# Kernel optimization log

Hardware: AMD Instinct MI355X
Metric: run time of the kernel (lower is better)

## Reference

```python
import jax, jax.numpy as jnp
import numpy as np

H = 16
DH = 64


def setup_inputs() -> dict:
    key = jax.random.key(0)
    ks = jax.random.split(key, 8)
    b, n, m, d = 2, 2048, 2048, 1024
    inner = H * DH  # 1024
    return {
        "x": jax.random.normal(ks[0], (b, n, d), jnp.float32),
        "mem_k": jax.random.normal(ks[1], (b, m, inner), jnp.float32),
        "mem_v": jax.random.normal(ks[2], (b, m, inner), jnp.float32),
        "Wq": jax.random.normal(ks[3], (d, inner), jnp.float32) * (d ** -0.5),
        "Wkv": jax.random.normal(ks[4], (d, 2 * inner), jnp.float32) * (d ** -0.5),
        "b_kv": jax.random.normal(ks[5], (2 * inner,), jnp.float32) * 0.02,
        "Wo": jax.random.normal(ks[6], (inner, d), jnp.float32) * (inner ** -0.5),
        "b_o": jax.random.normal(ks[7], (d,), jnp.float32) * 0.02,
    }


def reference(x, mem_k, mem_v, Wq, Wkv, b_kv, Wo, b_o):
    b, n, d = x.shape
    scale = DH ** -0.5
    q = (x @ Wq) * scale                       # [b, n, h*dh]
    self_k, self_v = jnp.split(x @ Wkv + b_kv, 2, axis=-1)
    k = jnp.concatenate([mem_k, self_k], axis=1)   # [b, j, h*dh]
    v = jnp.concatenate([mem_v, self_v], axis=1)

    def split_heads(t):
        return t.reshape(b, t.shape[1], H, DH).transpose(0, 2, 1, 3)  # b h n d

    q, k, v = map(split_heads, (q, k, v))
    sim = jnp.einsum('bhid,bhjd->bhij', q, k)  # [b, h, n, j]
    i, j = sim.shape[-2:]
    # causal mask: query i may attend to keys up to position (j - i) + i
    causal_mask = jnp.triu(jnp.ones((i, j), dtype=bool), k=j - i + 1)
    mask_value = -jnp.finfo(sim.dtype).max
    sim = jnp.where(causal_mask[None, None], mask_value, sim)
    attn = jax.nn.softmax(sim, axis=-1)
    out = jnp.einsum('bhij,bhjd->bhid', attn, v)
    out = out.transpose(0, 2, 1, 3).reshape(b, n, H * DH)
    return out @ Wo + b_o
```

## Files before the change

### kernel.cpp

```cpp
#include <hip/hip_runtime.h>
#include <stdint.h>

typedef __bf16 bf16x8 __attribute__((ext_vector_type(8)));
typedef _Float16 f16x8 __attribute__((ext_vector_type(8)));
typedef float f32x4 __attribute__((ext_vector_type(4)));
typedef float f32x16 __attribute__((ext_vector_type(16)));

constexpr int Mm = 2048;
constexpr float QSCALE = 0.18033688011112042f;

__device__ __forceinline__ float exp2_fast(float x) {
  return __builtin_amdgcn_exp2f(x);
}

__device__ __forceinline__ uint16_t f2bf(float f) {
  union { float f; uint32_t u; } v; v.f = f;
  return (uint16_t)((v.u + 0x7FFFu + ((v.u >> 16) & 1u)) >> 16);
}
__device__ __forceinline__ uint32_t pack2(float a, float b) {
  return (uint32_t)f2bf(a) | ((uint32_t)f2bf(b) << 16);
}
__device__ __forceinline__ uint32_t pkrtz(float a, float b) {
  auto h2 = __builtin_amdgcn_cvt_pkrtz(a, b);
  return __builtin_bit_cast(uint32_t, h2);
}
__device__ __forceinline__ uint16_t f2h(float f) {
  _Float16 h = (_Float16)f;
  return __builtin_bit_cast(uint16_t, h);
}

__device__ __forceinline__ void async16(const void* g, void* l) {
  __builtin_amdgcn_global_load_lds(
      (__attribute__((address_space(1))) uint32_t*)g,
      (__attribute__((address_space(3))) uint32_t*)l, 16, 0, 0);
}

__device__ __forceinline__ bf16x8 frag64(const uint16_t* base, int row, int chunk) {
  return *(const bf16x8*)(base + row * 64 + chunk * 8);
}
__device__ __forceinline__ f16x8 frag64h(const uint16_t* base, int row, int chunk) {
  return *(const f16x8*)(base + row * 64 + chunk * 8);
}

__global__ __launch_bounds__(256) void prep_kernel(
    const float* __restrict__ x, const float* __restrict__ mem_k,
    const float* __restrict__ mem_v, const float* __restrict__ Wq,
    const float* __restrict__ Wkv, const float* __restrict__ Wo,
    uint16_t* __restrict__ Xb, uint16_t* __restrict__ WallT,
    uint16_t* __restrict__ WoT, uint16_t* __restrict__ Kh,
    uint16_t* __restrict__ VhT) {
  __shared__ float tile[64][65];
  __shared__ uint16_t vtile[64 * 66];
  const int tid = threadIdx.x;
  int blk = blockIdx.x;

  if (blk < 1024) {
    const float4* x4 = (const float4*)x;
    for (int it = 0; it < 4; ++it) {
      int idx4 = blk * 1024 + it * 256 + tid;
      float4 v = x4[idx4];
      uint2 w; w.x = pack2(v.x, v.y); w.y = pack2(v.z, v.w);
      ((uint2*)Xb)[idx4] = w;
    }
    return;
  }
  blk -= 1024;
  if (blk < 1024) {
    const float* src; uint16_t* dst; int ld, colbase, n0, k0;
    if (blk < 768) {
      int nt = blk >> 4, kt = blk & 15;
      n0 = nt * 64; k0 = kt * 64;
      if (n0 < 1024) { src = Wq; ld = 1024; colbase = n0; }
      else           { src = Wkv; ld = 2048; colbase = n0 - 1024; }
      dst = WallT;
    } else {
      int b2 = blk - 768;
      int nt = b2 >> 4, kt = b2 & 15;
      n0 = nt * 64; k0 = kt * 64;
      src = Wo; ld = 1024; colbase = n0; dst = WoT;
    }
    int r = tid >> 4, c = (tid & 15) * 4;
    for (int it = 0; it < 4; ++it) {
      int rr = r + it * 16;
      float4 v = *(const float4*)(src + (size_t)(k0 + rr) * ld + colbase + c);
      tile[rr][c] = v.x; tile[rr][c + 1] = v.y;
      tile[rr][c + 2] = v.z; tile[rr][c + 3] = v.w;
    }
    __syncthreads();
    for (int it = 0; it < 4; ++it) {
      int rn = r + it * 16;
      uint2 w;
      w.x = pack2(tile[c][rn], tile[c + 1][rn]);
      w.y = pack2(tile[c + 2][rn], tile[c + 3][rn]);
      *(uint2*)(dst + (size_t)(n0 + rn) * 1024 + k0 + c) = w;
    }
    return;
  }
  blk -= 1024;
  if (blk < 1024) {
    const float4* s4 = (const float4*)mem_k;
    for (int it = 0; it < 4; ++it) {
      int idx4 = blk * 1024 + it * 256 + tid;
      int e = idx4 * 4;
      int b = e >> 21;
      int rem = e & ((1 << 21) - 1);
      int m = rem >> 10;
      int cc = rem & 1023;
      int h = cc >> 6, dh = cc & 63;
      float4 v = s4[idx4];
      uint2 w; w.x = pack2(v.x, v.y); w.y = pack2(v.z, v.w);
      *(uint2*)(Kh + (((size_t)(b * 16 + h) * 4096) + m) * 64 + dh) = w;
    }
    return;
  }
  blk -= 1024;
  {
    const int b = blk >> 9, h = (blk >> 5) & 15, m0 = (blk & 31) * 64;
    const float4* s4 = (const float4*)mem_v;
    for (int it = 0; it < 4; ++it) {
      int idx = it * 256 + tid;
      int r = idx >> 4, d4 = (idx & 15) * 4;
      float4 v = s4[(size_t)(b * 2048 + m0 + r) * 256 + h * 16 + (d4 >> 2)];
      *(uint32_t*)&vtile[r * 66 + d4]     = pkrtz(v.x, v.y);
      *(uint32_t*)&vtile[r * 66 + d4 + 2] = pkrtz(v.z, v.w);
    }
    __syncthreads();
    int d = tid & 63;
    for (int half = 0; half < 2; ++half) {
      int mg = (tid >> 6) + half * 4;
      uint32_t w[4];
      for (int p = 0; p < 4; ++p) {
        uint32_t lo = vtile[(mg * 8 + 2 * p) * 66 + d];
        uint32_t hi = vtile[(mg * 8 + 2 * p + 1) * 66 + d];
        w[p] = lo | (hi << 16);
      }
      *(uint4*)&VhT[((size_t)((b * 16 + h) * 64) + d) * 4096 + m0 + mg * 8] =
          *(uint4*)w;
    }
  }
}

template <int MODE>
__global__ __launch_bounds__(256) void gemm_kernel(
    const uint16_t* __restrict__ A, const uint16_t* __restrict__ Bt,
    const float* __restrict__ bias, uint16_t* __restrict__ Qh,
    uint16_t* __restrict__ Kh, uint16_t* __restrict__ VhT,
    float* __restrict__ Out) {
  constexpr int K = 1024;
  constexpr int SS = 136;
  const int m0 = blockIdx.x * 128, n0 = blockIdx.y * 128;
  const int tid = threadIdx.x;
  const int wave = tid >> 6, lane = tid & 63;
  const int lhi = lane >> 4, llo = lane & 15;
  const int wm = (wave >> 1) * 64, wn = (wave & 1) * 64;

  __shared__ uint16_t sh[MODE == 0 ? 128 * SS : 128 * 128];
  uint16_t* As = sh;
  uint16_t* Bs = sh + 128 * 64;

  f32x4 acc[4][4] = {};

  for (int kt = 0; kt < K / 64; ++kt) {
    __syncthreads();
    for (int c = 0; c < 4; ++c) {
      int cl = (wave * 4 + c) * 64 + lane;
      int row = cl >> 3;
      int ch = cl & 7;
      async16(A + (size_t)(m0 + row) * K + kt * 64 + ch * 8, As + cl * 8);
      async16(Bt + (size_t)(n0 + row) * K + kt * 64 + ch * 8, Bs + cl * 8);
    }
    __syncthreads();
    for (int ks = 0; ks < 2; ++ks) {
      bf16x8 af[4], bfr[4];
      for (int mt = 0; mt < 4; ++mt) af[mt] = frag64(As, wm + mt * 16 + llo, ks * 4 + lhi);
      for (int nt = 0; nt < 4; ++nt) bfr[nt] = frag64(Bs, wn + nt * 16 + llo, ks * 4 + lhi);
      for (int mt = 0; mt < 4; ++mt)
        for (int nt = 0; nt < 4; ++nt)
          acc[mt][nt] = __builtin_amdgcn_mfma_f32_16x16x32_bf16(af[mt], bfr[nt], acc[mt][nt], 0, 0, 0);
    }
  }

  if (MODE == 0) {
    const int region = n0 >> 10;
    __syncthreads();
    for (int nt = 0; nt < 4; ++nt) {
      int cloc = wn + nt * 16 + llo;
      int col = n0 + cloc;
      float badd = (region == 0) ? 0.f : bias[col - 1024];
      for (int mt = 0; mt < 4; ++mt) {
        int rloc = wm + mt * 16 + lhi * 4;
        for (int reg = 0; reg < 4; ++reg) {
          float v = acc[mt][nt][reg];
          v = (region == 0) ? v * QSCALE : v + badd;
          if (region == 2) sh[cloc * SS + rloc + reg] = f2h(v);
          else             sh[(rloc + reg) * SS + cloc] = f2bf(v);
        }
      }
    }
    __syncthreads();
    if (region == 2) {
      const int rl = (tid & 15) * 8;
      for (int it = 0; it < 8; ++it) {
        int cloc = (tid >> 4) + it * 16;
        int col = n0 + cloc;
        int cc = col - 2048, h = cc >> 6, dh = cc & 63;
        int r = m0 + rl;
        int b = r >> 11, n = r & 2047;
        uint4 w = *(const uint4*)&sh[cloc * SS + rl];
        *(uint4*)&VhT[((size_t)((b * 16 + h) * 64) + dh) * 4096 + 2048 + n] = w;
      }
    } else {
      const int cl16 = (tid & 15) * 8;
      const int col = n0 + cl16;
      for (int it = 0; it < 8; ++it) {
        int rloc = (tid >> 4) + it * 16;
        int r = m0 + rloc;
        int b = r >> 11, n = r & 2047;
        uint4 w = *(const uint4*)&sh[rloc * SS + cl16];
        if (region == 0) {
          int h = col >> 6, dh = col & 63;
          *(uint4*)&Qh[(((size_t)(b * 16 + h) * 2048) + n) * 64 + dh] = w;
        } else {
          int cc = col - 1024, h = cc >> 6, dh = cc & 63;
          *(uint4*)&Kh[(((size_t)(b * 16 + h) * 4096) + 2048 + n) * 64 + dh] = w;
        }
      }
    }
  } else {
    for (int nt = 0; nt < 4; ++nt) {
      int col = n0 + wn + nt * 16 + llo;
      float bo = bias[col];
      for (int mt = 0; mt < 4; ++mt) {
        int rbase = m0 + wm + mt * 16 + lhi * 4;
        for (int reg = 0; reg < 4; ++reg)
          Out[(size_t)(rbase + reg) * 1024 + col] = acc[mt][nt][reg] + bo;
      }
    }
  }
}

__global__ __launch_bounds__(256, 2) void attn_kernel(
    const uint16_t* __restrict__ Qh, const uint16_t* __restrict__ Kh,
    const uint16_t* __restrict__ VhT, uint16_t* __restrict__ AO) {
  const int bh = blockIdx.x;
  const int qt = 15 - blockIdx.y;
  const int tid = threadIdx.x;
  const int wave = tid >> 6, lane = tid & 63;
  const int lo5 = lane & 31, hi = lane >> 5;
  const int i0 = qt * 128;
  const int iw = i0 + wave * 32;
  const int swz5 = lo5 & 7;

  __shared__ uint16_t Ks[2][64 * 64];
  __shared__ uint16_t Vt[2][64 * 64];

  bf16x8 qf[4];
  {
    const uint16_t* Qw = Qh + ((size_t)bh * 2048 + iw + lo5) * 64;
#pragma unroll
    for (int kstep = 0; kstep < 4; ++kstep)
      qf[kstep] = *(const bf16x8*)(Qw + kstep * 16 + hi * 8);
  }

  const uint16_t* Kbh = Kh + (size_t)bh * 4096 * 64;
  const uint16_t* Vbh = VhT + (size_t)bh * 64 * 4096;

  f16x8 onesf;
#pragma unroll
  for (int i = 0; i < 8; ++i) onesf[i] = (_Float16)1.0f;

  f32x16 o0 = {}, o1 = {};
  f32x16 lacc = {};

  const int nkt = 34 + 2 * qt;

  auto stage = [&](int buf, int t) {
    const int k0 = t * 64;
    for (int c = 0; c < 2; ++c) {
      int cl = (wave * 2 + c) * 64 + lane;
      int row = cl >> 3, ch = cl & 7;
      int chs = ch ^ (row & 7);
      async16(Kbh + (size_t)(k0 + row) * 64 + chs * 8, &Ks[buf][cl * 8]);
      async16(Vbh + (size_t)row * 4096 + k0 + chs * 8, &Vt[buf][cl * 8]);
    }
  };

  stage(0, 0);

  for (int t = 0; t < nkt; ++t) {
    const int cur = t & 1;
    const int k0 = t * 64;
    __syncthreads();
    if (t + 1 < nkt) stage(cur ^ 1, t + 1);

#pragma unroll
    for (int mblk = 0; mblk < 2; ++mblk) {
      f32x16 s = {};
      __builtin_amdgcn_s_setprio(1);
#pragma unroll
      for (int kstep = 0; kstep < 4; ++kstep) {
        bf16x8 kf = frag64(&Ks[cur][0], mblk * 32 + lo5, (2 * kstep + hi) ^ swz5);
        s = __builtin_amdgcn_mfma_f32_32x32x16_bf16(kf, qf[kstep], s, 0, 0, 0);
      }
      __builtin_amdgcn_s_setprio(0);

      if (k0 + mblk * 32 + 31 > Mm + iw) {
        const int lim = Mm + iw + lo5 - k0 - mblk * 32;
#pragma unroll
        for (int r = 0; r < 16; ++r) {
          int kl = (r & 3) + 8 * (r >> 2) + 4 * hi;
          if (kl > lim) s[r] = -INFINITY;
        }
      }

      uint32_t c[8];
#pragma unroll
      for (int w = 0; w < 8; ++w)
        c[w] = pkrtz(exp2_fast(s[2 * w]), exp2_fast(s[2 * w + 1]));

#pragma unroll
      for (int kk2 = 0; kk2 < 2; ++kk2) {
        uint32_t w0 = c[4 * kk2 + 0], w2 = c[4 * kk2 + 2];
        uint32_t w1 = c[4 * kk2 + 1], w3 = c[4 * kk2 + 3];
        asm volatile("v_permlane32_swap_b32 %0, %1" : "+v"(w0), "+v"(w2));
        asm volatile("v_permlane32_swap_b32 %0, %1" : "+v"(w1), "+v"(w3));
        uint4 fw; fw.x = w0; fw.y = w1; fw.z = w2; fw.w = w3;
        f16x8 pa = __builtin_bit_cast(f16x8, fw);
        const int kk = mblk * 2 + kk2;
        __builtin_amdgcn_s_setprio(1);
        {
          f16x8 vf0 = frag64h(&Vt[cur][0], lo5,      (2 * kk + hi) ^ swz5);
          f16x8 vf1 = frag64h(&Vt[cur][0], 32 + lo5, (2 * kk + hi) ^ swz5);
          o0 = __builtin_amdgcn_mfma_f32_32x32x16_f16(pa, vf0, o0, 0, 0, 0);
          o1 = __builtin_amdgcn_mfma_f32_32x32x16_f16(pa, vf1, o1, 0, 0, 0);
          lacc = __builtin_amdgcn_mfma_f32_32x32x16_f16(pa, onesf, lacc, 0, 0, 0);
        }
        __builtin_amdgcn_s_setprio(0);
      }
    }
  }

  const int b = bh >> 4, h = bh & 15;
  uint16_t* Es = &Ks[0][0];
  __syncthreads();
#pragma unroll
  for (int r = 0; r < 16; ++r) {
    float inv = 1.0f / lacc[r];
    int q = wave * 32 + (r & 3) + 8 * (r >> 2) + 4 * hi;
    Es[q * 64 + lo5]      = f2bf(o0[r] * inv);
    Es[q * 64 + 32 + lo5] = f2bf(o1[r] * inv);
  }
  __syncthreads();
  {
    int row = tid >> 1, c32 = (tid & 1) * 32;
    size_t base = ((size_t)(b * 2048) + i0 + row) * 1024 + h * 64 + c32;
    *(uint4*)&AO[base]      = *(const uint4*)&Es[row * 64 + c32];
    *(uint4*)&AO[base + 8]  = *(const uint4*)&Es[row * 64 + c32 + 8];
    *(uint4*)&AO[base + 16] = *(const uint4*)&Es[row * 64 + c32 + 16];
    *(uint4*)&AO[base + 24] = *(const uint4*)&Es[row * 64 + c32 + 24];
  }
}

extern "C" void kernel_launch(void* const* d_in, const int* in_sizes, int n_in,
                              void* d_out, int out_size, void* d_ws,
                              size_t ws_size, hipStream_t stream) {
  const float* x     = (const float*)d_in[0];
  const float* mem_k = (const float*)d_in[1];
  const float* mem_v = (const float*)d_in[2];
  const float* Wq    = (const float*)d_in[3];
  const float* Wkv   = (const float*)d_in[4];
  const float* b_kv  = (const float*)d_in[5];
  const float* Wo    = (const float*)d_in[6];
  const float* b_o   = (const float*)d_in[7];
  float* out = (float*)d_out;

  char* ws = (char*)d_ws;
  uint16_t* Xb    = (uint16_t*)(ws);
  uint16_t* WallT = (uint16_t*)(ws + (8ull << 20));
  uint16_t* WoT   = (uint16_t*)(ws + (14ull << 20));
  uint16_t* Qh    = (uint16_t*)(ws + (16ull << 20));
  uint16_t* Kh    = (uint16_t*)(ws + (24ull << 20));
  uint16_t* VhT   = (uint16_t*)(ws + (40ull << 20));
  uint16_t* AO    = (uint16_t*)(ws + (56ull << 20));

  prep_kernel<<<4096, 256, 0, stream>>>(x, mem_k, mem_v, Wq, Wkv, Wo,
                                        Xb, WallT, WoT, Kh, VhT);
  gemm_kernel<0><<<dim3(32, 24), 256, 0, stream>>>(Xb, WallT, b_kv,
                                                   Qh, Kh, VhT, nullptr);
  attn_kernel<<<dim3(32, 16), 256, 0, stream>>>(Qh, Kh, VhT, AO);
  gemm_kernel<1><<<dim3(32, 8), 256, 0, stream>>>(AO, WoT, b_o,
                                                  nullptr, nullptr, nullptr, out);
}
```

Measured before the change: 264.5 us.

## Split attention waves by query pair and key parity, reuse K fragments

Each wave now handles 64 query rows (two 32-row blocks) instead of 32. The four waves are split into two query groups and two key-tile parities, and each iteration stages 128 keys into double-buffered LDS. Every K fragment read from LDS feeds two score MFMAs, and every V fragment feeds two output MFMAs, which cuts LDS traffic per unit of compute. The two parity partials are merged through LDS (fp32 outputs and row sums) before normalization. The cost is higher register pressure, double the LDS footprint, and an extra reduction phase at the end.

```diff
diff --git a/kernel.cpp b/kernel.cpp
--- a/kernel.cpp
+++ b/kernel.cpp
@@ -247,19 +247,22 @@
   const int tid = threadIdx.x;
   const int wave = tid >> 6, lane = tid & 63;
   const int lo5 = lane & 31, hi = lane >> 5;
+  const int qg = wave & 1, kp = wave >> 1;
   const int i0 = qt * 128;
-  const int iw = i0 + wave * 32;
   const int swz5 = lo5 & 7;
 
-  __shared__ uint16_t Ks[2][64 * 64];
-  __shared__ uint16_t Vt[2][64 * 64];
-
-  bf16x8 qf[4];
+  __shared__ uint16_t Ks[2][2][64 * 64];
+  __shared__ uint16_t Vt[2][2][64 * 64];
+
+  bf16x8 qf0[4], qf1[4];
   {
-    const uint16_t* Qw = Qh + ((size_t)bh * 2048 + iw + lo5) * 64;
-#pragma unroll
-    for (int kstep = 0; kstep < 4; ++kstep)
-      qf[kstep] = *(const bf16x8*)(Qw + kstep * 16 + hi * 8);
+    const uint16_t* Qw0 = Qh + ((size_t)bh * 2048 + i0 + qg * 64 + lo5) * 64;
+    const uint16_t* Qw1 = Qw0 + 32 * 64;
+#pragma unroll
+    for (int k = 0; k < 4; ++k) {
+      qf0[k] = *(const bf16x8*)(Qw0 + k * 16 + hi * 8);
+      qf1[k] = *(const bf16x8*)(Qw1 + k * 16 + hi * 8);
+    }
   }
 
   const uint16_t* Kbh = Kh + (size_t)bh * 4096 * 64;
@@ -269,86 +272,138 @@
 #pragma unroll
   for (int i = 0; i < 8; ++i) onesf[i] = (_Float16)1.0f;
 
-  f32x16 o0 = {}, o1 = {};
-  f32x16 lacc = {};
-
-  const int nkt = 34 + 2 * qt;
-
-  auto stage = [&](int buf, int t) {
-    const int k0 = t * 64;
-    for (int c = 0; c < 2; ++c) {
-      int cl = (wave * 2 + c) * 64 + lane;
-      int row = cl >> 3, ch = cl & 7;
-      int chs = ch ^ (row & 7);
-      async16(Kbh + (size_t)(k0 + row) * 64 + chs * 8, &Ks[buf][cl * 8]);
-      async16(Vbh + (size_t)row * 4096 + k0 + chs * 8, &Vt[buf][cl * 8]);
+  f32x16 o00 = {}, o01 = {}, o10 = {}, o11 = {};
+  f32x16 l0v = {}, l1v = {};
+
+  const int npairs = 17 + qt;
+
+  auto stage = [&](int buf, int u_) {
+    const int arr = wave >> 1;
+    const int par = wave & 1;
+    const int kk0 = u_ * 128 + par * 64;
+    uint16_t* dstb = arr == 0 ? &Ks[buf][par][0] : &Vt[buf][par][0];
+#pragma unroll
+    for (int c = 0; c < 8; ++c) {
+      int row = c * 8 + (lane >> 3);
+      int chs = (lane & 7) ^ (row & 7);
+      const uint16_t* src = arr == 0
+          ? Kbh + (size_t)(kk0 + row) * 64 + chs * 8
+          : Vbh + (size_t)row * 4096 + kk0 + chs * 8;
+      async16(src, dstb + c * 512);
     }
   };
 
   stage(0, 0);
 
-  for (int t = 0; t < nkt; ++t) {
-    const int cur = t & 1;
-    const int k0 = t * 64;
-    __syncthreads();
-    if (t + 1 < nkt) stage(cur ^ 1, t + 1);
+  const int iw0 = i0 + qg * 64;
+  const int iw1 = iw0 + 32;
+
+  for (int u = 0; u < npairs; ++u) {
+    const int cur = u & 1;
+    __syncthreads();
+    if (u + 1 < npairs) stage(cur ^ 1, u + 1);
+
+    const int k0t = (2 * u + kp) * 64;
+    const uint16_t* Kt = &Ks[cur][kp][0];
+    const uint16_t* Vtt = &Vt[cur][kp][0];
 
 #pragma unroll
     for (int mblk = 0; mblk < 2; ++mblk) {
-      f32x16 s = {};
+      f32x16 s0v = {}, s1v = {};
       __builtin_amdgcn_s_setprio(1);
 #pragma unroll
       for (int kstep = 0; kstep < 4; ++kstep) {
-        bf16x8 kf = frag64(&Ks[cur][0], mblk * 32 + lo5, (2 * kstep + hi) ^ swz5);
-        s = __builtin_amdgcn_mfma_f32_32x32x16_bf16(kf, qf[kstep], s, 0, 0, 0);
+        bf16x8 kf = frag64(Kt, mblk * 32 + lo5, (2 * kstep + hi) ^ swz5);
+        s0v = __builtin_amdgcn_mfma_f32_32x32x16_bf16(kf, qf0[kstep], s0v, 0, 0, 0);
+        s1v = __builtin_amdgcn_mfma_f32_32x32x16_bf16(kf, qf1[kstep], s1v, 0, 0, 0);
       }
       __builtin_amdgcn_s_setprio(0);
 
-      if (k0 + mblk * 32 + 31 > Mm + iw) {
-        const int lim = Mm + iw + lo5 - k0 - mblk * 32;
+      if (k0t + mblk * 32 + 31 > Mm + iw0) {
+        const int lim = Mm + iw0 + lo5 - k0t - mblk * 32;
 #pragma unroll
         for (int r = 0; r < 16; ++r) {
           int kl = (r & 3) + 8 * (r >> 2) + 4 * hi;
-          if (kl > lim) s[r] = -INFINITY;
+          if (kl > lim) s0v[r] = -INFINITY;
         }
       }
-
-      uint32_t c[8];
-#pragma unroll
-      for (int w = 0; w < 8; ++w)
-        c[w] = pkrtz(exp2_fast(s[2 * w]), exp2_fast(s[2 * w + 1]));
+      if (k0t + mblk * 32 + 31 > Mm + iw1) {
+        const int lim = Mm + iw1 + lo5 - k0t - mblk * 32;
+#pragma unroll
+        for (int r = 0; r < 16; ++r) {
+          int kl = (r & 3) + 8 * (r >> 2) + 4 * hi;
+          if (kl > lim) s1v[r] = -INFINITY;
+        }
+      }
+
+      uint32_t c0[8], c1[8];
+#pragma unroll
+      for (int w = 0; w < 8; ++w) {
+        c0[w] = pkrtz(exp2_fast(s0v[2 * w]), exp2_fast(s0v[2 * w + 1]));
+        c1[w] = pkrtz(exp2_fast(s1v[2 * w]), exp2_fast(s1v[2 * w + 1]));
+      }
 
 #pragma unroll
       for (int kk2 = 0; kk2 < 2; ++kk2) {
-        uint32_t w0 = c[4 * kk2 + 0], w2 = c[4 * kk2 + 2];
-        uint32_t w1 = c[4 * kk2 + 1], w3 = c[4 * kk2 + 3];
-        asm volatile("v_permlane32_swap_b32 %0, %1" : "+v"(w0), "+v"(w2));
-        asm volatile("v_permlane32_swap_b32 %0, %1" : "+v"(w1), "+v"(w3));
-        uint4 fw; fw.x = w0; fw.y = w1; fw.z = w2; fw.w = w3;
-        f16x8 pa = __builtin_bit_cast(f16x8, fw);
+        uint32_t a0 = c0[4 * kk2 + 0], a2 = c0[4 * kk2 + 2];
+        uint32_t a1 = c0[4 * kk2 + 1], a3 = c0[4 * kk2 + 3];
+        asm volatile("v_permlane32_swap_b32 %0, %1" : "+v"(a0), "+v"(a2));
+        asm volatile("v_permlane32_swap_b32 %0, %1" : "+v"(a1), "+v"(a3));
+        uint4 fwa; fwa.x = a0; fwa.y = a1; fwa.z = a2; fwa.w = a3;
+        f16x8 pa0 = __builtin_bit_cast(f16x8, fwa);
+        uint32_t b0 = c1[4 * kk2 + 0], b2 = c1[4 * kk2 + 2];
+        uint32_t b1 = c1[4 * kk2 + 1], b3 = c1[4 * kk2 + 3];
+        asm volatile("v_permlane32_swap_b32 %0, %1" : "+v"(b0), "+v"(b2));
+        asm volatile("v_permlane32_swap_b32 %0, %1" : "+v"(b1), "+v"(b3));
+        uint4 fwb; fwb.x = b0; fwb.y = b1; fwb.z = b2; fwb.w = b3;
+        f16x8 pa1 = __builtin_bit_cast(f16x8, fwb);
+
         const int kk = mblk * 2 + kk2;
+        f16x8 vf0 = frag64h(Vtt, lo5,      (2 * kk + hi) ^ swz5);
+        f16x8 vf1 = frag64h(Vtt, 32 + lo5, (2 * kk + hi) ^ swz5);
         __builtin_amdgcn_s_setprio(1);
-        {
-          f16x8 vf0 = frag64h(&Vt[cur][0], lo5,      (2 * kk + hi) ^ swz5);
-          f16x8 vf1 = frag64h(&Vt[cur][0], 32 + lo5, (2 * kk + hi) ^ swz5);
-          o0 = __builtin_amdgcn_mfma_f32_32x32x16_f16(pa, vf0, o0, 0, 0, 0);
-          o1 = __builtin_amdgcn_mfma_f32_32x32x16_f16(pa, vf1, o1, 0, 0, 0);
-          lacc = __builtin_amdgcn_mfma_f32_32x32x16_f16(pa, onesf, lacc, 0, 0, 0);
-        }
+        o00 = __builtin_amdgcn_mfma_f32_32x32x16_f16(pa0, vf0, o00, 0, 0, 0);
+        o01 = __builtin_amdgcn_mfma_f32_32x32x16_f16(pa0, vf1, o01, 0, 0, 0);
+        o10 = __builtin_amdgcn_mfma_f32_32x32x16_f16(pa1, vf0, o10, 0, 0, 0);
+        o11 = __builtin_amdgcn_mfma_f32_32x32x16_f16(pa1, vf1, o11, 0, 0, 0);
+        l0v = __builtin_amdgcn_mfma_f32_32x32x16_f16(pa0, onesf, l0v, 0, 0, 0);
+        l1v = __builtin_amdgcn_mfma_f32_32x32x16_f16(pa1, onesf, l1v, 0, 0, 0);
         __builtin_amdgcn_s_setprio(0);
       }
     }
   }
 
   const int b = bh >> 4, h = bh & 15;
-  uint16_t* Es = &Ks[0][0];
+  float* F = (float*)&Ks[0][0][0];
+  float* L = (float*)&Vt[1][0][0];
+  uint16_t* Es = &Vt[0][0][0];
+
   __syncthreads();
-#pragma unroll
-  for (int r = 0; r < 16; ++r) {
-    float inv = 1.0f / lacc[r];
-    int q = wave * 32 + (r & 3) + 8 * (r >> 2) + 4 * hi;
-    Es[q * 64 + lo5]      = f2bf(o0[r] * inv);
-    Es[q * 64 + 32 + lo5] = f2bf(o1[r] * inv);
+  if (kp == 1) {
+#pragma unroll
+    for (int r = 0; r < 16; ++r) {
+      int q0 = qg * 64 + (r & 3) + 8 * (r >> 2) + 4 * hi;
+      int q1 = q0 + 32;
+      F[q0 * 64 + lo5]      = o00[r];
+      F[q0 * 64 + 32 + lo5] = o01[r];
+      F[q1 * 64 + lo5]      = o10[r];
+      F[q1 * 64 + 32 + lo5] = o11[r];
+      if (lo5 == 0) { L[q0] = l0v[r]; L[q1] = l1v[r]; }
+    }
+  }
+  __syncthreads();
+  if (kp == 0) {
+#pragma unroll
+    for (int r = 0; r < 16; ++r) {
+      int q0 = qg * 64 + (r & 3) + 8 * (r >> 2) + 4 * hi;
+      int q1 = q0 + 32;
+      float inv0 = 1.0f / (l0v[r] + L[q0]);
+      float inv1 = 1.0f / (l1v[r] + L[q1]);
+      Es[q0 * 64 + lo5]      = f2bf((o00[r] + F[q0 * 64 + lo5]) * inv0);
+      Es[q0 * 64 + 32 + lo5] = f2bf((o01[r] + F[q0 * 64 + 32 + lo5]) * inv0);
+      Es[q1 * 64 + lo5]      = f2bf((o10[r] + F[q1 * 64 + lo5]) * inv1);
+      Es[q1 * 64 + 32 + lo5] = f2bf((o11[r] + F[q1 * 64 + 32 + lo5]) * inv1);
+    }
   }
   __syncthreads();
   {
```

New measurement: 260.2 us. About the same (-1.6%).
